# Performance work log

Hardware: AMD Instinct MI355X
Metric: run time of the kernel (lower is better)

Reference implementation:

```python
import jax, jax.numpy as jnp
import numpy as np

N, DEG, B, DM, NH, DOUT = 100000, 32, 8192, 256, 4, 128
EPS = 1e-6

def rmsnorm(x, w):
    return x * jax.lax.rsqrt(jnp.mean(x * x, axis=-1, keepdims=True) + EPS) * w

def setup_inputs():
    key = jax.random.key(0)
    ks = jax.random.split(key, 16)
    s = 0.02
    H = jax.random.normal(ks[0], (N, DM), jnp.float32)
    # CSR-friendly graph: every node has exactly DEG out-neighbors (src already sorted)
    src = jnp.repeat(jnp.arange(N, dtype=jnp.int32), DEG)
    dst = jax.random.randint(ks[1], (N * DEG,), 0, N, dtype=jnp.int32)
    edge_index = jnp.stack([src, dst])
    centers = jax.random.randint(ks[2], (B,), 0, N, dtype=jnp.int32)
    target = jax.random.normal(ks[3], (N, DOUT), jnp.float32)
    p = lambda k, sh: jax.random.normal(k, sh, jnp.float32) * s
    return dict(
        H=H, edge_index=edge_index, centers=centers, target=target, max_deg=DEG,
        ln_in_w=jnp.ones((DM,), jnp.float32), ln1_w=jnp.ones((DM,), jnp.float32), ln2_w=jnp.ones((DM,), jnp.float32),
        w_qkv=p(ks[4], (3 * DM, DM)), b_qkv=jnp.zeros((3 * DM,), jnp.float32),
        w_o=p(ks[5], (DM, DM)), b_o=jnp.zeros((DM,), jnp.float32),
        w_gate=p(ks[6], (DM, DM)), w_up=p(ks[7], (DM, DM)), w_down=p(ks[8], (DM, DM)),
        w_head=p(ks[9], (DOUT, DM)), b_head=jnp.zeros((DOUT,), jnp.float32),
    )

def _forward(H, target, ln_in_w, ln1_w, ln2_w, w_qkv, b_qkv, w_o, b_o, w_gate, w_up, w_down, w_head, b_head, edge_index, centers, max_deg):
    n, d = H.shape
    Bc = centers.shape[0]
    src, dst = edge_index[0], edge_index[1]
    # CSR-like sort by source (assume_undirected=True: no reverse edges added)
    order = jnp.argsort(src)
    dst_s = dst[order]
    counts = jnp.bincount(src, length=n)
    row_ptr = jnp.concatenate([jnp.zeros((1,), counts.dtype), jnp.cumsum(counts)])
    starts = row_ptr[centers]
    deg = jnp.minimum(row_ptr[centers + 1] - starts, max_deg)  # cap at max_neighbors
    pos = jnp.arange(max_deg)[None, :]
    mask = pos < deg[:, None]                                   # [B, max_deg]
    idx_in = jnp.clip(starts[:, None] + pos, 0, dst_s.shape[0] - 1)
    nbrs = jnp.where(mask, dst_s[idx_in], -1)                   # padded neighbor ids
    idx_mat = jnp.concatenate([centers[:, None].astype(nbrs.dtype), nbrs], axis=1)  # [B, L]
    kpm = idx_mat == -1                                         # key padding mask
    X = H[jnp.maximum(idx_mat, 0)]                              # [B, L, d] star pack
    X = rmsnorm(X, ln_in_w)
    X = jnp.where(kpm[..., None], 0.0, X)
    # encoder block (num_layers = 1): RMSNorm -> MHA -> residual -> RMSNorm -> gated MLP -> residual
    xn = rmsnorm(X, ln1_w)
    qkv = xn @ w_qkv.T + b_qkv
    q, k, v = jnp.split(qkv, 3, axis=-1)
    hd = d // NH
    L = 1 + max_deg
    sh = lambda t: t.reshape(Bc, L, NH, hd).transpose(0, 2, 1, 3)
    qh, kh, vh = sh(q), sh(k), sh(v)
    scores = jnp.einsum('bhqc,bhkc->bhqk', qh, kh) * np.float32(1.0 / np.sqrt(hd))
    scores = jnp.where(kpm[:, None, None, :], -jnp.inf, scores)
    attn = jax.nn.softmax(scores, axis=-1)
    ao = jnp.einsum('bhqk,bhkc->bhqc', attn, vh).transpose(0, 2, 1, 3).reshape(Bc, L, d)
    X = X + ao @ w_o.T + b_o
    xn2 = rmsnorm(X, ln2_w)
    Z = X + (jax.nn.silu(xn2 @ w_gate.T) * (xn2 @ w_up.T)) @ w_down.T
    # per-pair MTP loss on frontier (neighbor) positions, mean_per_center reduction
    y_hat = Z[:, 1:] @ w_head.T + b_head                        # [B, max_deg, DOUT]
    y_true = target[jnp.maximum(nbrs, 0)]
    err = jnp.mean((y_hat - y_true) ** 2, axis=-1)
    err = jnp.where(mask, err, 0.0)
    cnt = jnp.maximum(deg.astype(err.dtype), 1.0)
    return jnp.mean(jnp.sum(err, axis=1) / cnt)

def reference(H, edge_index, centers, target, max_deg, ln_in_w, ln1_w, ln2_w, w_qkv, b_qkv, w_o, b_o, w_gate, w_up, w_down, w_head, b_head):
    return _forward(H, target, ln_in_w, ln1_w, ln2_w, w_qkv, b_qkv, w_o, b_o, w_gate, w_up, w_down, w_head, b_head, edge_index, centers, max_deg)
```

## Files before the change

### kernel.cpp

```cpp
#include <hip/hip_runtime.h>

#define DM 256
#define NH 4
#define HD 64
#define DEG 32
#define LQ 33
#define DOUT 128
#define NTHREADS 256

typedef __attribute__((ext_vector_type(8))) short bf8v;
typedef __attribute__((ext_vector_type(4))) float f4v;

__device__ __forceinline__ float b2f(unsigned short u){ union{unsigned int i;float f;}v; v.i=((unsigned int)u)<<16; return v.f; }
__device__ __forceinline__ unsigned short f2b(float f){
  union{float f;unsigned int i;}v; v.f=f;
  unsigned int r=v.i+0x7FFFu+((v.i>>16)&1u);
  return (unsigned short)(r>>16);
}
__device__ __forceinline__ float wred(float x){
  #pragma unroll
  for (int o=32;o>=1;o>>=1) x += __shfl_xor(x,o,64);
  return x;
}

__device__ __forceinline__ int swz(int r, int c){ return r*DM + (((c>>3) ^ (r&7))<<3) + (c&7); }
__device__ __forceinline__ int swzV(int r, int c){ return r*HD + (((c>>3) ^ (r&7))<<3) + (c&7); }

template<bool BF>
__device__ __forceinline__ bf8v wfrag(const float* Wf, const unsigned short* Wb,
                                      const float* fold1, const float* fold2, int row, int e){
  if constexpr (BF) {
    return *(const bf8v*)(Wb + (size_t)row*DM + e);
  } else {
    const float* p = Wf + (size_t)row*DM + e;
    float4 a = *(const float4*)p;
    float4 b = *(const float4*)(p+4);
    if (fold1) {
      const float4 fa = *(const float4*)(fold1+e), fb = *(const float4*)(fold1+e+4);
      a.x*=fa.x; a.y*=fa.y; a.z*=fa.z; a.w*=fa.w;
      b.x*=fb.x; b.y*=fb.y; b.z*=fb.z; b.w*=fb.w;
    }
    if (fold2) {
      const float4 fa = *(const float4*)(fold2+e), fb = *(const float4*)(fold2+e+4);
      a.x*=fa.x; a.y*=fa.y; a.z*=fa.z; a.w*=fa.w;
      b.x*=fb.x; b.y*=fb.y; b.z*=fb.z; b.w*=fb.w;
    }
    bf8v r;
    r[0]=(short)f2b(a.x); r[1]=(short)f2b(a.y); r[2]=(short)f2b(a.z); r[3]=(short)f2b(a.w);
    r[4]=(short)f2b(b.x); r[5]=(short)f2b(b.y); r[6]=(short)f2b(b.z); r[7]=(short)f2b(b.w);
    return r;
  }
}

__device__ __forceinline__ f4v mfma16(bf8v a, bf8v b, f4v c){
  return __builtin_amdgcn_mfma_f32_16x16x32_bf16(a, b, c, 0, 0, 0);
}

#define U_Q  0
#define U_K  3072
#define U_VT 6144
#define RB   12288
#define U_SZ 24576

template<bool WBF16>
__global__ __launch_bounds__(NTHREADS, 2) void smtp_center(
    const float* __restrict__ H,
    const int* __restrict__ dstE,
    const int* __restrict__ centers,
    const float* __restrict__ target,
    const float* __restrict__ ln_in_w,
    const float* __restrict__ ln1_w,
    const float* __restrict__ ln2_w,
    const float* __restrict__ w_qkv,
    const float* __restrict__ b_qkv,
    const float* __restrict__ w_o,
    const float* __restrict__ b_o,
    const float* __restrict__ w_gate,
    const float* __restrict__ w_up,
    const float* __restrict__ w_down,
    const float* __restrict__ w_head,
    const float* __restrict__ b_head,
    const unsigned short* __restrict__ wb,
    float* __restrict__ partial)
{
  __shared__ __align__(16) unsigned short U[U_SZ];
  __shared__ __align__(16) unsigned short Hb[48*DM];
  __shared__ float sS0[48];
  __shared__ float sS1[48];
  __shared__ float sRowSum[48*4];
  __shared__ int sIdx[48];
  __shared__ float sRed[4];

  const unsigned short* wbQKV = wb;
  const unsigned short* wbO   = wb + 196608;
  const unsigned short* wbG   = wb + 262144;
  const unsigned short* wbU   = wb + 327680;
  const unsigned short* wbD   = wb + 393216;
  const unsigned short* wbH   = wb + 458752;

  const int tid  = threadIdx.x;
  const int lane = tid & 63;
  const int wave = tid >> 6;
  const int bid  = blockIdx.x;
  const int l15  = lane & 15;
  const int l16  = (lane >> 4) * 8;
  const int rsub = (lane >> 4) * 4;

  if (tid < 48) {
    int ctr = centers[bid];
    sIdx[tid] = (tid == 0) ? ctr : (tid < 1+DEG ? dstE[(size_t)ctr*DEG + (tid-1)] : 0);
  }
  __syncthreads();

  for (int r = wave; r < 48; r += 4) {
    if (r < LQ) {
      const float4 x4 = ((const float4*)(H + (size_t)sIdx[r]*DM))[lane];
      const float4 wi = ((const float4*)ln_in_w)[lane];
      ushort4 hb; hb.x=f2b(x4.x); hb.y=f2b(x4.y); hb.z=f2b(x4.z); hb.w=f2b(x4.w);
      *(ushort4*)(Hb + swz(r, lane*4)) = hb;
      float ssh = x4.x*x4.x + x4.y*x4.y + x4.z*x4.z + x4.w*x4.w;
      const float w0 = x4.x*wi.x, w1 = x4.y*wi.y, w2 = x4.z*wi.z, w3 = x4.w*wi.w;
      float ssw = w0*w0 + w1*w1 + w2*w2 + w3*w3;
      ssh = wred(ssh);
      ssw = wred(ssw);
      if (lane == 0) {
        const float rsH = rsqrtf(ssh*(1.f/DM) + 1e-6f);
        const float rs2 = rsqrtf(rsH*rsH*ssw*(1.f/DM) + 1e-6f);
        sS0[r] = rsH;
        sS1[r] = rsH*rs2;
      }
    } else {
      ushort4 z4; z4.x=0; z4.y=0; z4.z=0; z4.w=0;
      *(ushort4*)(Hb + swz(r, lane*4)) = z4;
      if (lane == 0) { sS0[r] = 0.f; sS1[r] = 0.f; }
    }
  }
  if (tid < 128) {
    const int d = tid >> 1;
    const int key = 48 + (tid & 1)*8;
    *(uint4*)&U[U_VT + swzV(d, key)] = make_uint4(0,0,0,0);
  }
  __syncthreads();

  float s1v[3][4];
  #pragma unroll
  for (int m = 0; m < 3; ++m)
    #pragma unroll
    for (int j = 0; j < 4; ++j)
      s1v[m][j] = sS1[m*16 + rsub + j];

  for (int h = 0; h < NH; ++h) {
    {
      int wrow[3], sect[3];
      #pragma unroll
      for (int t3 = 0; t3 < 3; ++t3) {
        const int t = wave*3 + t3;
        sect[t3] = t >> 2;
        wrow[t3] = sect[t3]*DM + h*HD + ((t*16 + l15) & 63);
      }
      f4v acc[3][3];
      #pragma unroll
      for (int t3 = 0; t3 < 3; ++t3)
        #pragma unroll
        for (int m = 0; m < 3; ++m)
          acc[t3][m] = (f4v){0.f,0.f,0.f,0.f};
      #pragma unroll
      for (int k = 0; k < 8; ++k) {
        bf8v aF[3];
        #pragma unroll
        for (int m = 0; m < 3; ++m)
          aF[m] = *(const bf8v*)(Hb + swz(m*16 + l15, k*32 + l16));
        #pragma unroll
        for (int t3 = 0; t3 < 3; ++t3) {
          const bf8v b = wfrag<WBF16>(w_qkv, wbQKV, ln_in_w, ln1_w, wrow[t3], k*32 + l16);
          #pragma unroll
          for (int m = 0; m < 3; ++m)
            acc[t3][m] = mfma16(aF[m], b, acc[t3][m]);
        }
      }
      #pragma unroll
      for (int t3 = 0; t3 < 3; ++t3) {
        const float bias = b_qkv[wrow[t3]];
        const int c = wrow[t3] & 63;
        if (sect[t3] == 2) {
          #pragma unroll
          for (int m = 0; m < 3; ++m)
            #pragma unroll
            for (int j = 0; j < 4; ++j)
              U[U_VT + swzV(c, m*16 + rsub + j)] = f2b(acc[t3][m][j]*s1v[m][j] + bias);
        } else {
          unsigned short* dstb = U + (sect[t3] ? U_K : U_Q);
          #pragma unroll
          for (int m = 0; m < 3; ++m)
            #pragma unroll
            for (int j = 0; j < 4; ++j)
              dstb[swzV(m*16 + rsub + j, c)] = f2b(acc[t3][m][j]*s1v[m][j] + bias);
        }
      }
    }
    __syncthreads();

    if (wave < 3) {
      f4v s3[3];
      s3[0] = (f4v){0.f,0.f,0.f,0.f}; s3[1] = s3[0]; s3[2] = s3[0];
      #pragma unroll
      for (int kk = 0; kk < 2; ++kk) {
        const bf8v a = *(const bf8v*)(U + U_Q + swzV(wave*16 + l15, kk*32 + l16));
        #pragma unroll
        for (int nk = 0; nk < 3; ++nk) {
          const bf8v bb = *(const bf8v*)(U + U_K + swzV(nk*16 + l15, kk*32 + l16));
          s3[nk] = mfma16(a, bb, s3[nk]);
        }
      }
      #pragma unroll
      for (int j = 0; j < 4; ++j) {
        const float v0 = s3[0][j]*0.125f;
        const float v1 = s3[1][j]*0.125f;
        const float v2 = (l15 >= 1) ? -INFINITY : s3[2][j]*0.125f;
        float mx = fmaxf(fmaxf(v0, v1), v2);
        mx = fmaxf(mx, __shfl_xor(mx, 1, 64));
        mx = fmaxf(mx, __shfl_xor(mx, 2, 64));
        mx = fmaxf(mx, __shfl_xor(mx, 4, 64));
        mx = fmaxf(mx, __shfl_xor(mx, 8, 64));
        const float e0 = __expf(v0 - mx), e1 = __expf(v1 - mx), e2 = __expf(v2 - mx);
        float den = e0 + e1 + e2;
        den += __shfl_xor(den, 1, 64);
        den += __shfl_xor(den, 2, 64);
        den += __shfl_xor(den, 4, 64);
        den += __shfl_xor(den, 8, 64);
        const float rn = 1.f / den;
        const int row = wave*16 + rsub + j;
        U[U_Q + swzV(row, 0*16 + l15)] = f2b(e0 * rn);
        U[U_Q + swzV(row, 1*16 + l15)] = f2b(e1 * rn);
        U[U_Q + swzV(row, 2*16 + l15)] = f2b(e2 * rn);
      }
    }
    __syncthreads();

    {
      f4v o4[3];
      o4[0] = (f4v){0.f,0.f,0.f,0.f}; o4[1] = o4[0]; o4[2] = o4[0];
      #pragma unroll
      for (int kk = 0; kk < 2; ++kk) {
        const bf8v bb = *(const bf8v*)(U + U_VT + swzV(wave*16 + l15, kk*32 + l16));
        #pragma unroll
        for (int mq = 0; mq < 3; ++mq) {
          const bf8v a = *(const bf8v*)(U + U_Q + swzV(mq*16 + l15, kk*32 + l16));
          o4[mq] = mfma16(a, bb, o4[mq]);
        }
      }
      #pragma unroll
      for (int mq = 0; mq < 3; ++mq)
        #pragma unroll
        for (int j = 0; j < 4; ++j)
          U[RB + swz(mq*16 + rsub + j, h*HD + wave*16 + l15)] = f2b(o4[mq][j]);
    }
    __syncthreads();
  }

  {
    f4v acc[3][4];
    #pragma unroll
    for (int t4 = 0; t4 < 4; ++t4) {
      const int col = wave*64 + t4*16 + l15;
      const float bo = b_o[col];
      const float wi = ln_in_w[col];
      #pragma unroll
      for (int m = 0; m < 3; ++m)
        #pragma unroll
        for (int j = 0; j < 4; ++j) {
          const int row = m*16 + rsub + j;
          acc[m][t4][j] = sS0[row]*b2f(Hb[swz(row, col)])*wi + bo;
        }
    }
    #pragma unroll
    for (int k = 0; k < 8; ++k) {
      bf8v aA[3];
      #pragma unroll
      for (int m = 0; m < 3; ++m)
        aA[m] = *(const bf8v*)(U + RB + swz(m*16 + l15, k*32 + l16));
      #pragma unroll
      for (int t4 = 0; t4 < 4; ++t4) {
        const int col = wave*64 + t4*16 + l15;
        const bf8v b = wfrag<WBF16>(w_o, wbO, nullptr, nullptr, col, k*32 + l16);
        #pragma unroll
        for (int m = 0; m < 3; ++m)
          acc[m][t4] = mfma16(aA[m], b, acc[m][t4]);
      }
    }
    #pragma unroll
    for (int m = 0; m < 3; ++m)
      #pragma unroll
      for (int j = 0; j < 4; ++j) {
        float p = 0.f;
        #pragma unroll
        for (int t4 = 0; t4 < 4; ++t4) p += acc[m][t4][j]*acc[m][t4][j];
        p += __shfl_xor(p, 1, 64);
        p += __shfl_xor(p, 2, 64);
        p += __shfl_xor(p, 4, 64);
        p += __shfl_xor(p, 8, 64);
        if (l15 == 0) sRowSum[(m*16 + rsub + j)*4 + wave] = p;
      }
    __syncthreads();
    #pragma unroll
    for (int t4 = 0; t4 < 4; ++t4) {
      const int col = wave*64 + t4*16 + l15;
      #pragma unroll
      for (int m = 0; m < 3; ++m)
        #pragma unroll
        for (int j = 0; j < 4; ++j)
          U[RB + swz(m*16 + rsub + j, col)] = f2b(acc[m][t4][j]);
    }
  }
  __syncthreads();

  #pragma unroll
  for (int p = 0; p < 2; ++p) {
    f4v aG[2][3], aU[2][3];
    #pragma unroll
    for (int tt = 0; tt < 2; ++tt)
      #pragma unroll
      for (int m = 0; m < 3; ++m) { aG[tt][m] = (f4v){0.f,0.f,0.f,0.f}; aU[tt][m] = aG[tt][m]; }
    #pragma unroll
    for (int k = 0; k < 8; ++k) {
      bf8v aF[3];
      #pragma unroll
      for (int m = 0; m < 3; ++m)
        aF[m] = *(const bf8v*)(U + RB + swz(m*16 + l15, k*32 + l16));
      #pragma unroll
      for (int tt = 0; tt < 2; ++tt) {
        const int col = wave*64 + (p*2 + tt)*16 + l15;
        const bf8v bg = wfrag<WBF16>(w_gate, wbG, ln2_w, nullptr, col, k*32 + l16);
        const bf8v bu = wfrag<WBF16>(w_up,   wbU, ln2_w, nullptr, col, k*32 + l16);
        #pragma unroll
        for (int m = 0; m < 3; ++m) {
          aG[tt][m] = mfma16(aF[m], bg, aG[tt][m]);
          aU[tt][m] = mfma16(aF[m], bu, aU[tt][m]);
        }
      }
    }
    #pragma unroll
    for (int tt = 0; tt < 2; ++tt) {
      const int col = wave*64 + (p*2 + tt)*16 + l15;
      #pragma unroll
      for (int m = 0; m < 3; ++m)
        #pragma unroll
        for (int j = 0; j < 4; ++j) {
          const int row = m*16 + rsub + j;
          const float tot = sRowSum[row*4+0] + sRowSum[row*4+1] + sRowSum[row*4+2] + sRowSum[row*4+3];
          const float rs3 = rsqrtf(tot*(1.f/DM) + 1e-6f);
          const float g = aG[tt][m][j]*rs3;
          const float uu = aU[tt][m][j]*rs3;
          const float v = (g / (1.f + __expf(-g))) * uu;
          U[swz(row, col)] = f2b(v);
        }
    }
  }
  __syncthreads();

  {
    f4v acc[3][4];
    #pragma unroll
    for (int t4 = 0; t4 < 4; ++t4) {
      const int col = wave*64 + t4*16 + l15;
      #pragma unroll
      for (int m = 0; m < 3; ++m)
        #pragma unroll
        for (int j = 0; j < 4; ++j)
          acc[m][t4][j] = b2f(U[RB + swz(m*16 + rsub + j, col)]);
    }
    #pragma unroll
    for (int k = 0; k < 8; ++k) {
      bf8v aM[3];
      #pragma unroll
      for (int m = 0; m < 3; ++m)
        aM[m] = *(const bf8v*)(U + swz(m*16 + l15, k*32 + l16));
      #pragma unroll
      for (int t4 = 0; t4 < 4; ++t4) {
        const int col = wave*64 + t4*16 + l15;
        const bf8v b = wfrag<WBF16>(w_down, wbD, nullptr, nullptr, col, k*32 + l16);
        #pragma unroll
        for (int m = 0; m < 3; ++m)
          acc[m][t4] = mfma16(aM[m], b, acc[m][t4]);
      }
    }
    #pragma unroll
    for (int t4 = 0; t4 < 4; ++t4) {
      const int col = wave*64 + t4*16 + l15;
      #pragma unroll
      for (int m = 0; m < 3; ++m)
        #pragma unroll
        for (int j = 0; j < 4; ++j)
          U[RB + swz(m*16 + rsub + j, col)] = f2b(acc[m][t4][j]);
    }
  }
  __syncthreads();

  float lsum = 0.f;
  {
    int cols[2]; f4v acc[2][2];
    #pragma unroll
    for (int t2 = 0; t2 < 2; ++t2) {
      cols[t2] = (wave*2 + t2)*16 + l15;
      const float bh = b_head[cols[t2]];
      acc[t2][0] = (f4v){bh,bh,bh,bh}; acc[t2][1] = acc[t2][0];
    }
    #pragma unroll
    for (int k = 0; k < 8; ++k) {
      bf8v aH[2];
      #pragma unroll
      for (int m = 0; m < 2; ++m)
        aH[m] = *(const bf8v*)(U + RB + swz(1 + m*16 + l15, k*32 + l16));
      #pragma unroll
      for (int t2 = 0; t2 < 2; ++t2) {
        const bf8v b = wfrag<WBF16>(w_head, wbH, nullptr, nullptr, cols[t2], k*32 + l16);
        #pragma unroll
        for (int m = 0; m < 2; ++m)
          acc[t2][m] = mfma16(aH[m], b, acc[t2][m]);
      }
    }
    #pragma unroll
    for (int t2 = 0; t2 < 2; ++t2)
      #pragma unroll
      for (int m = 0; m < 2; ++m)
        #pragma unroll
        for (int j = 0; j < 4; ++j) {
          const int row = 1 + m*16 + rsub + j;
          const float tv = target[(size_t)sIdx[row]*DOUT + cols[t2]];
          const float d = acc[t2][m][j] - tv;
          lsum += d*d;
        }
  }
  lsum = wred(lsum);
  if (lane == 0) sRed[wave] = lsum;
  __syncthreads();
  if (tid == 0)
    partial[bid] = (sRed[0]+sRed[1]+sRed[2]+sRed[3]) * (1.f/(DEG*DOUT));
}

__global__ void cvt_w(const float* __restrict__ qkv, const float* __restrict__ o,
                      const float* __restrict__ g, const float* __restrict__ u,
                      const float* __restrict__ dn, const float* __restrict__ hd,
                      const float* __restrict__ lin, const float* __restrict__ l1,
                      const float* __restrict__ l2,
                      unsigned short* __restrict__ out)
{
  const int i = blockIdx.x*NTHREADS + threadIdx.x;
  const int e = i*2;
  if (e >= 491520) return;
  const float* src; int off;
  float f0 = 1.f, f1 = 1.f;
  if      (e < 196608){ src=qkv; off=e;        const int c=off&255; f0=lin[c]*l1[c]; f1=lin[c+1]*l1[c+1]; }
  else if (e < 262144){ src=o;  off=e-196608; }
  else if (e < 327680){ src=g;  off=e-262144;  const int c=off&255; f0=l2[c]; f1=l2[c+1]; }
  else if (e < 393216){ src=u;  off=e-327680;  const int c=off&255; f0=l2[c]; f1=l2[c+1]; }
  else if (e < 458752){ src=dn; off=e-393216; }
  else                { src=hd; off=e-458752; }
  const float2 v = *(const float2*)(src + off);
  const unsigned int pk = (unsigned int)f2b(v.x*f0) | ((unsigned int)f2b(v.y*f1) << 16);
  *(unsigned int*)(out + e) = pk;
}

__global__ void smtp_reduce(const float* __restrict__ partial, int B, float* __restrict__ out)
{
  __shared__ float sRed[4];
  const int tid = threadIdx.x;
  float s = 0.f;
  for (int i = tid; i < B; i += NTHREADS) s += partial[i];
  s = wred(s);
  if ((tid & 63) == 0) sRed[tid>>6] = s;
  __syncthreads();
  if (tid == 0) out[0] = (sRed[0]+sRed[1]+sRed[2]+sRed[3]) / (float)B;
}

extern "C" void kernel_launch(void* const* d_in, const int* in_sizes, int n_in,
                              void* d_out, int out_size, void* d_ws, size_t ws_size,
                              hipStream_t stream) {
  const float* H        = (const float*)d_in[0];
  const int*   edge     = (const int*)d_in[1];
  const int*   centers  = (const int*)d_in[2];
  const float* target   = (const float*)d_in[3];
  const float* ln_in_w  = (const float*)d_in[5];
  const float* ln1_w    = (const float*)d_in[6];
  const float* ln2_w    = (const float*)d_in[7];
  const float* w_qkv    = (const float*)d_in[8];
  const float* b_qkv    = (const float*)d_in[9];
  const float* w_o      = (const float*)d_in[10];
  const float* b_o      = (const float*)d_in[11];
  const float* w_gate   = (const float*)d_in[12];
  const float* w_up     = (const float*)d_in[13];
  const float* w_down   = (const float*)d_in[14];
  const float* w_head   = (const float*)d_in[15];
  const float* b_head   = (const float*)d_in[16];

  const int B = in_sizes[2];
  const int E = in_sizes[1] / 2;
  const int* dstE = edge + E;

  const size_t WB_ELEMS = 491520;
  const size_t NEED = WB_ELEMS*2 + (size_t)B*4;
  const bool useBf = (ws_size >= NEED);

  if (useBf) {
    unsigned short* wb = (unsigned short*)d_ws;
    float* partial = (float*)((char*)d_ws + WB_ELEMS*2);
    cvt_w<<<960, NTHREADS, 0, stream>>>(w_qkv, w_o, w_gate, w_up, w_down, w_head,
                                        ln_in_w, ln1_w, ln2_w, wb);
    smtp_center<true><<<B, NTHREADS, 0, stream>>>(H, dstE, centers, target, ln_in_w, ln1_w, ln2_w,
        w_qkv, b_qkv, w_o, b_o, w_gate, w_up, w_down, w_head, b_head, wb, partial);
    smtp_reduce<<<1, NTHREADS, 0, stream>>>(partial, B, (float*)d_out);
  } else {
    float* partial = (float*)d_ws;
    smtp_center<false><<<B, NTHREADS, 0, stream>>>(H, dstE, centers, target, ln_in_w, ln1_w, ln2_w,
        w_qkv, b_qkv, w_o, b_o, w_gate, w_up, w_down, w_head, b_head, (const unsigned short*)d_ws, partial);
    smtp_reduce<<<1, NTHREADS, 0, stream>>>(partial, B, (float*)d_out);
  }
}
```

Measured before the change: 1.301 ms.

## Transpose MFMA operands so accumulators hold contiguous columns for vectorized epilogues

The post-attention GEMMs (out-proj, gate/up, down, head) now swap the MFMA A/B operands, putting weights in A and activations in B. Each lane's four accumulator values then cover four consecutive output features of one token instead of four tokens of one feature. Epilogue stores become packed 8-byte bf16 writes via v_cvt_pk_bf16_f32, and residual, bias and target loads become float4/ushort4 vector loads. RMSNorm row sums need only two shuffles instead of four, and the rsqrt is computed once per token rather than per element. This cuts scalar LDS and global traffic in the epilogues and adds some risk of LDS bank conflicts with the new access pattern.

```diff
diff --git a/kernel.cpp b/kernel.cpp
--- a/kernel.cpp
+++ b/kernel.cpp
@@ -23,8 +23,16 @@
   return x;
 }
 
-__device__ __forceinline__ int swz(int r, int c){ return r*DM + (((c>>3) ^ (r&7))<<3) + (c&7); }
+__device__ __forceinline__ int swz (int r, int c){ return r*DM + (((c>>3) ^ (r&7))<<3) + (c&7); }
 __device__ __forceinline__ int swzV(int r, int c){ return r*HD + (((c>>3) ^ (r&7))<<3) + (c&7); }
+
+__device__ __forceinline__ void packw(unsigned short* dst, float a0, float a1, float a2, float a3){
+  unsigned int lo, hi;
+  asm("v_cvt_pk_bf16_f32 %0,%1,%2" : "=v"(lo) : "v"(a0), "v"(a1));
+  asm("v_cvt_pk_bf16_f32 %0,%1,%2" : "=v"(hi) : "v"(a2), "v"(a3));
+  uint2 u; u.x = lo; u.y = hi;
+  *(uint2*)dst = u;
+}
 
 template<bool BF>
 __device__ __forceinline__ bf8v wfrag(const float* Wf, const unsigned short* Wb,
@@ -136,9 +144,8 @@
     }
   }
   if (tid < 128) {
-    const int d = tid >> 1;
-    const int key = 48 + (tid & 1)*8;
-    *(uint4*)&U[U_VT + swzV(d, key)] = make_uint4(0,0,0,0);
+    const int d = tid >> 1, ch = 6 + (tid & 1);
+    *(uint4*)&U[U_VT + d*HD + ((ch ^ (d&7))<<3)] = make_uint4(0,0,0,0);
   }
   __syncthreads();
 
@@ -258,59 +265,59 @@
     __syncthreads();
   }
 
+
   {
-    f4v acc[3][4];
+    f4v acc[4][3];
     #pragma unroll
     for (int t4 = 0; t4 < 4; ++t4) {
-      const int col = wave*64 + t4*16 + l15;
-      const float bo = b_o[col];
-      const float wi = ln_in_w[col];
+      const int db = (wave*4 + t4)*16 + rsub;
+      const float4 wi4 = *(const float4*)(ln_in_w + db);
+      const float4 bo4 = *(const float4*)(b_o + db);
+      #pragma unroll
+      for (int m = 0; m < 3; ++m) {
+        const int tok = m*16 + l15;
+        const ushort4 x0 = *(const ushort4*)&Hb[swz(tok, db)];
+        const float s0 = sS0[tok];
+        acc[t4][m] = (f4v){ b2f(x0.x)*s0*wi4.x + bo4.x, b2f(x0.y)*s0*wi4.y + bo4.y,
+                            b2f(x0.z)*s0*wi4.z + bo4.z, b2f(x0.w)*s0*wi4.w + bo4.w };
+      }
+    }
+    #pragma unroll
+    for (int k = 0; k < 8; ++k) {
+      bf8v bA[3];
       #pragma unroll
       for (int m = 0; m < 3; ++m)
-        #pragma unroll
-        for (int j = 0; j < 4; ++j) {
-          const int row = m*16 + rsub + j;
-          acc[m][t4][j] = sS0[row]*b2f(Hb[swz(row, col)])*wi + bo;
-        }
-    }
-    #pragma unroll
-    for (int k = 0; k < 8; ++k) {
-      bf8v aA[3];
+        bA[m] = *(const bf8v*)(U + RB + swz(m*16 + l15, k*32 + l16));
+      #pragma unroll
+      for (int t4 = 0; t4 < 4; ++t4) {
+        const bf8v w = wfrag<WBF16>(w_o, wbO, nullptr, nullptr, (wave*4 + t4)*16 + l15, k*32 + l16);
+        #pragma unroll
+        for (int m = 0; m < 3; ++m)
+          acc[t4][m] = mfma16(w, bA[m], acc[t4][m]);
+      }
+    }
+    float p[3];
+    #pragma unroll
+    for (int m = 0; m < 3; ++m) {
+      p[m] = 0.f;
+      #pragma unroll
+      for (int t4 = 0; t4 < 4; ++t4)
+        #pragma unroll
+        for (int j = 0; j < 4; ++j) p[m] += acc[t4][m][j]*acc[t4][m][j];
+      p[m] += __shfl_xor(p[m], 16, 64);
+      p[m] += __shfl_xor(p[m], 32, 64);
+    }
+    if (lane < 16) {
+      #pragma unroll
+      for (int m = 0; m < 3; ++m) sRowSum[(m*16 + l15)*4 + wave] = p[m];
+    }
+    __syncthreads();
+    #pragma unroll
+    for (int t4 = 0; t4 < 4; ++t4)
       #pragma unroll
       for (int m = 0; m < 3; ++m)
-        aA[m] = *(const bf8v*)(U + RB + swz(m*16 + l15, k*32 + l16));
-      #pragma unroll
-      for (int t4 = 0; t4 < 4; ++t4) {
-        const int col = wave*64 + t4*16 + l15;
-        const bf8v b = wfrag<WBF16>(w_o, wbO, nullptr, nullptr, col, k*32 + l16);
-        #pragma unroll
-        for (int m = 0; m < 3; ++m)
-          acc[m][t4] = mfma16(aA[m], b, acc[m][t4]);
-      }
-    }
-    #pragma unroll
-    for (int m = 0; m < 3; ++m)
-      #pragma unroll
-      for (int j = 0; j < 4; ++j) {
-        float p = 0.f;
-        #pragma unroll
-        for (int t4 = 0; t4 < 4; ++t4) p += acc[m][t4][j]*acc[m][t4][j];
-        p += __shfl_xor(p, 1, 64);
-        p += __shfl_xor(p, 2, 64);
-        p += __shfl_xor(p, 4, 64);
-        p += __shfl_xor(p, 8, 64);
-        if (l15 == 0) sRowSum[(m*16 + rsub + j)*4 + wave] = p;
-      }
-    __syncthreads();
-    #pragma unroll
-    for (int t4 = 0; t4 < 4; ++t4) {
-      const int col = wave*64 + t4*16 + l15;
-      #pragma unroll
-      for (int m = 0; m < 3; ++m)
-        #pragma unroll
-        for (int j = 0; j < 4; ++j)
-          U[RB + swz(m*16 + rsub + j, col)] = f2b(acc[m][t4][j]);
-    }
+        packw(&U[RB + swz(m*16 + l15, (wave*4 + t4)*16 + rsub)],
+              acc[t4][m][0], acc[t4][m][1], acc[t4][m][2], acc[t4][m][3]);
   }
   __syncthreads();
 
@@ -323,113 +330,115 @@
       for (int m = 0; m < 3; ++m) { aG[tt][m] = (f4v){0.f,0.f,0.f,0.f}; aU[tt][m] = aG[tt][m]; }
     #pragma unroll
     for (int k = 0; k < 8; ++k) {
-      bf8v aF[3];
+      bf8v bX[3];
       #pragma unroll
       for (int m = 0; m < 3; ++m)
-        aF[m] = *(const bf8v*)(U + RB + swz(m*16 + l15, k*32 + l16));
+        bX[m] = *(const bf8v*)(U + RB + swz(m*16 + l15, k*32 + l16));
       #pragma unroll
       for (int tt = 0; tt < 2; ++tt) {
-        const int col = wave*64 + (p*2 + tt)*16 + l15;
-        const bf8v bg = wfrag<WBF16>(w_gate, wbG, ln2_w, nullptr, col, k*32 + l16);
-        const bf8v bu = wfrag<WBF16>(w_up,   wbU, ln2_w, nullptr, col, k*32 + l16);
+        const int wr = (wave*4 + p*2 + tt)*16 + l15;
+        const bf8v bg = wfrag<WBF16>(w_gate, wbG, ln2_w, nullptr, wr, k*32 + l16);
+        const bf8v bu = wfrag<WBF16>(w_up,   wbU, ln2_w, nullptr, wr, k*32 + l16);
         #pragma unroll
         for (int m = 0; m < 3; ++m) {
-          aG[tt][m] = mfma16(aF[m], bg, aG[tt][m]);
-          aU[tt][m] = mfma16(aF[m], bu, aU[tt][m]);
+          aG[tt][m] = mfma16(bg, bX[m], aG[tt][m]);
+          aU[tt][m] = mfma16(bu, bX[m], aU[tt][m]);
         }
       }
     }
-    #pragma unroll
-    for (int tt = 0; tt < 2; ++tt) {
-      const int col = wave*64 + (p*2 + tt)*16 + l15;
+    float rs3c[3];
+    #pragma unroll
+    for (int m = 0; m < 3; ++m) {
+      const int tok = m*16 + l15;
+      const float tot = sRowSum[tok*4+0] + sRowSum[tok*4+1] + sRowSum[tok*4+2] + sRowSum[tok*4+3];
+      rs3c[m] = rsqrtf(tot*(1.f/DM) + 1e-6f);
+    }
+    #pragma unroll
+    for (int tt = 0; tt < 2; ++tt)
+      #pragma unroll
+      for (int m = 0; m < 3; ++m) {
+        float vv[4];
+        #pragma unroll
+        for (int j = 0; j < 4; ++j) {
+          const float g = aG[tt][m][j]*rs3c[m];
+          const float u = aU[tt][m][j]*rs3c[m];
+          vv[j] = (g / (1.f + __expf(-g))) * u;
+        }
+        packw(&U[swz(m*16 + l15, (wave*4 + p*2 + tt)*16 + rsub)], vv[0], vv[1], vv[2], vv[3]);
+      }
+  }
+  __syncthreads();
+
+  {
+    f4v acc[4][3];
+    #pragma unroll
+    for (int t4 = 0; t4 < 4; ++t4) {
+      const int db = (wave*4 + t4)*16 + rsub;
+      #pragma unroll
+      for (int m = 0; m < 3; ++m) {
+        const ushort4 x1 = *(const ushort4*)&U[RB + swz(m*16 + l15, db)];
+        acc[t4][m] = (f4v){ b2f(x1.x), b2f(x1.y), b2f(x1.z), b2f(x1.w) };
+      }
+    }
+    #pragma unroll
+    for (int k = 0; k < 8; ++k) {
+      bf8v bM[3];
       #pragma unroll
       for (int m = 0; m < 3; ++m)
-        #pragma unroll
-        for (int j = 0; j < 4; ++j) {
-          const int row = m*16 + rsub + j;
-          const float tot = sRowSum[row*4+0] + sRowSum[row*4+1] + sRowSum[row*4+2] + sRowSum[row*4+3];
-          const float rs3 = rsqrtf(tot*(1.f/DM) + 1e-6f);
-          const float g = aG[tt][m][j]*rs3;
-          const float uu = aU[tt][m][j]*rs3;
-          const float v = (g / (1.f + __expf(-g))) * uu;
-          U[swz(row, col)] = f2b(v);
-        }
-    }
-  }
-  __syncthreads();
-
-  {
-    f4v acc[3][4];
-    #pragma unroll
-    for (int t4 = 0; t4 < 4; ++t4) {
-      const int col = wave*64 + t4*16 + l15;
+        bM[m] = *(const bf8v*)(U + swz(m*16 + l15, k*32 + l16));
+      #pragma unroll
+      for (int t4 = 0; t4 < 4; ++t4) {
+        const bf8v w = wfrag<WBF16>(w_down, wbD, nullptr, nullptr, (wave*4 + t4)*16 + l15, k*32 + l16);
+        #pragma unroll
+        for (int m = 0; m < 3; ++m)
+          acc[t4][m] = mfma16(w, bM[m], acc[t4][m]);
+      }
+    }
+    #pragma unroll
+    for (int t4 = 0; t4 < 4; ++t4)
       #pragma unroll
       for (int m = 0; m < 3; ++m)
-        #pragma unroll
-        for (int j = 0; j < 4; ++j)
-          acc[m][t4][j] = b2f(U[RB + swz(m*16 + rsub + j, col)]);
-    }
-    #pragma unroll
-    for (int k = 0; k < 8; ++k) {
-      bf8v aM[3];
-      #pragma unroll
-      for (int m = 0; m < 3; ++m)
-        aM[m] = *(const bf8v*)(U + swz(m*16 + l15, k*32 + l16));
-      #pragma unroll
-      for (int t4 = 0; t4 < 4; ++t4) {
-        const int col = wave*64 + t4*16 + l15;
-        const bf8v b = wfrag<WBF16>(w_down, wbD, nullptr, nullptr, col, k*32 + l16);
-        #pragma unroll
-        for (int m = 0; m < 3; ++m)
-          acc[m][t4] = mfma16(aM[m], b, acc[m][t4]);
-      }
-    }
-    #pragma unroll
-    for (int t4 = 0; t4 < 4; ++t4) {
-      const int col = wave*64 + t4*16 + l15;
-      #pragma unroll
-      for (int m = 0; m < 3; ++m)
-        #pragma unroll
-        for (int j = 0; j < 4; ++j)
-          U[RB + swz(m*16 + rsub + j, col)] = f2b(acc[m][t4][j]);
-    }
+        packw(&U[RB + swz(m*16 + l15, (wave*4 + t4)*16 + rsub)],
+              acc[t4][m][0], acc[t4][m][1], acc[t4][m][2], acc[t4][m][3]);
   }
   __syncthreads();
 
   float lsum = 0.f;
   {
-    int cols[2]; f4v acc[2][2];
+    f4v acc[2][2];
     #pragma unroll
     for (int t2 = 0; t2 < 2; ++t2) {
-      cols[t2] = (wave*2 + t2)*16 + l15;
-      const float bh = b_head[cols[t2]];
-      acc[t2][0] = (f4v){bh,bh,bh,bh}; acc[t2][1] = acc[t2][0];
+      const float4 bh4 = *(const float4*)(b_head + (wave*2 + t2)*16 + rsub);
+      #pragma unroll
+      for (int m = 0; m < 2; ++m)
+        acc[t2][m] = (f4v){ bh4.x, bh4.y, bh4.z, bh4.w };
     }
     #pragma unroll
     for (int k = 0; k < 8; ++k) {
-      bf8v aH[2];
+      bf8v bZ[2];
       #pragma unroll
       for (int m = 0; m < 2; ++m)
-        aH[m] = *(const bf8v*)(U + RB + swz(1 + m*16 + l15, k*32 + l16));
+        bZ[m] = *(const bf8v*)(U + RB + swz(1 + m*16 + l15, k*32 + l16));
       #pragma unroll
       for (int t2 = 0; t2 < 2; ++t2) {
-        const bf8v b = wfrag<WBF16>(w_head, wbH, nullptr, nullptr, cols[t2], k*32 + l16);
+        const bf8v w = wfrag<WBF16>(w_head, wbH, nullptr, nullptr, (wave*2 + t2)*16 + l15, k*32 + l16);
         #pragma unroll
         for (int m = 0; m < 2; ++m)
-          acc[t2][m] = mfma16(aH[m], b, acc[t2][m]);
+          acc[t2][m] = mfma16(w, bZ[m], acc[t2][m]);
       }
     }
     #pragma unroll
     for (int t2 = 0; t2 < 2; ++t2)
       #pragma unroll
-      for (int m = 0; m < 2; ++m)
-        #pragma unroll
-        for (int j = 0; j < 4; ++j) {
-          const int row = 1 + m*16 + rsub + j;
-          const float tv = target[(size_t)sIdx[row]*DOUT + cols[t2]];
-          const float d = acc[t2][m][j] - tv;
-          lsum += d*d;
-        }
+      for (int m = 0; m < 2; ++m) {
+        const int tok = 1 + m*16 + l15;
+        const float4 tv = *(const float4*)&target[(size_t)sIdx[tok]*DOUT + (wave*2 + t2)*16 + rsub];
+        const float d0 = acc[t2][m][0] - tv.x;
+        const float d1 = acc[t2][m][1] - tv.y;
+        const float d2 = acc[t2][m][2] - tv.z;
+        const float d3 = acc[t2][m][3] - tv.w;
+        lsum += d0*d0 + d1*d1 + d2*d2 + d3*d3;
+      }
   }
   lsum = wred(lsum);
   if (lane == 0) sRed[wave] = lsum;
```

Measured after the change: 1.129 ms. 1.15x faster.
